# Kernel tuning notes

Measured on AMD Instinct MI355X. Metric: run time of the kernel, lower is better.

## Reference

```python
import jax, jax.numpy as jnp
import numpy as np

B, N, D = 4, 16384, 1024
RANK, NUM_Q = 16, 8
SPARSITY = 0.1
K = max(1, int(N * SPARSITY))  # 1638


def setup_inputs() -> dict:
    key = jax.random.key(0)
    k1, k2, k3 = jax.random.split(key, 3)
    x = jax.random.normal(k1, (B, N, D), dtype=jnp.float32)
    Wk = jax.random.normal(k2, (RANK, D), dtype=jnp.float32)
    queries = jax.random.normal(k3, (NUM_Q, RANK), dtype=jnp.float32)
    return {"x": x, "Wk": Wk, "queries": queries}


def reference(x, Wk, queries):
    # k_proj: [b, n, d] @ [d, rank] -> [b, n, rank]
    keys = jnp.einsum("bnd,rd->bnr", x, Wk)
    # scores: [q, r] x [b, n, r] -> [b, q, n]
    scores = jnp.einsum("qr,bnr->bqn", queries, keys)
    # max over queries -> [b, n]
    token_scores = scores.max(axis=1)
    # eval mode: no jitter noise
    _, indices = jax.lax.top_k(token_scores, K)  # [b, K]
    indices = jnp.sort(indices, axis=-1)
    return indices
```

## Files before the change

kernel.cpp:

```cpp
#include <hip/hip_runtime.h>
#include <stdint.h>

#define B_ 4
#define N_ 16384
#define D_ 1024
#define RANK_ 16
#define NUMQ_ 8
#define KSEL_ 1638

__global__ __launch_bounds__(256) void wq_kernel(const float* __restrict__ Wk,
                                                 const float* __restrict__ queries,
                                                 float* __restrict__ Wq) {
    int i = blockIdx.x * 256 + threadIdx.x;
    if (i >= NUMQ_ * D_) return;
    int q = i >> 10;
    int d = i & (D_ - 1);
    float acc = 0.f;
#pragma unroll
    for (int r = 0; r < RANK_; ++r)
        acc += queries[q * RANK_ + r] * Wk[r * D_ + d];
    Wq[i] = acc;
}

#define TOK 4
__global__ __launch_bounds__(256) void score_kernel(const float* __restrict__ x,
                                                    const float* __restrict__ Wq,
                                                    float* __restrict__ scores) {
    __shared__ float sWq[NUMQ_ * D_];
    for (int i = threadIdx.x; i < NUMQ_ * D_; i += 256)
        sWq[i] = Wq[i];
    __syncthreads();

    const int lane = threadIdx.x & 63;
    const int wave = threadIdx.x >> 6;
    const int gw = blockIdx.x * 4 + wave;
    const int numWaves = gridDim.x * 4;
    const int totalTok = B_ * N_;

    for (int t0 = gw * TOK; t0 < totalTok; t0 += numWaves * TOK) {
        float acc[TOK][NUMQ_];
#pragma unroll
        for (int t = 0; t < TOK; ++t)
#pragma unroll
            for (int q = 0; q < NUMQ_; ++q) acc[t][q] = 0.f;

#pragma unroll
        for (int j = 0; j < 4; ++j) {
            const int off = j * 256 + lane * 4;
            float4 xv[TOK];
#pragma unroll
            for (int t = 0; t < TOK; ++t)
                xv[t] = *(const float4*)(x + (size_t)(t0 + t) * D_ + off);
#pragma unroll
            for (int q = 0; q < NUMQ_; ++q) {
                float4 w = *(const float4*)(sWq + q * D_ + off);
#pragma unroll
                for (int t = 0; t < TOK; ++t) {
                    acc[t][q] += xv[t].x * w.x;
                    acc[t][q] += xv[t].y * w.y;
                    acc[t][q] += xv[t].z * w.z;
                    acc[t][q] += xv[t].w * w.w;
                }
            }
        }

#pragma unroll
        for (int t = 0; t < TOK; ++t) {
            float m = -3.0e38f;
#pragma unroll
            for (int q = 0; q < NUMQ_; ++q) {
                float v = acc[t][q];
#pragma unroll
                for (int s = 32; s > 0; s >>= 1)
                    v += __shfl_xor(v, s, 64);
                m = fmaxf(m, v);
            }
            if (lane == 0) scores[t0 + t] = m;
        }
    }
}

__global__ __launch_bounds__(256) void topk_kernel(const float* __restrict__ scores,
                                                   int* __restrict__ out) {
    __shared__ uint32_t sKeys[N_];
    __shared__ uint32_t hist[256];
    __shared__ uint32_t sGT[256];
    __shared__ uint32_t sEQ[256];
    __shared__ uint32_t sPrefix, sR;

    const int b = blockIdx.x;
    const int tid = threadIdx.x;
    const float* s = scores + b * N_;

    for (int i = tid; i < N_; i += 256) {
        uint32_t u = __float_as_uint(s[i]);
        u = (u & 0x80000000u) ? ~u : (u | 0x80000000u);
        sKeys[i] = u;
    }
    __syncthreads();

    uint32_t prefix = 0;
    uint32_t R = KSEL_;

    for (int shift = 24; shift >= 0; shift -= 8) {
        hist[tid] = 0;
        __syncthreads();
        const uint32_t maskHi = (shift == 24) ? 0u : (0xFFFFFFFFu << (shift + 8));
        for (int i = tid; i < N_; i += 256) {
            uint32_t u = sKeys[i];
            if ((u & maskHi) == prefix)
                atomicAdd(&hist[(u >> shift) & 255u], 1u);
        }
        __syncthreads();
        if (tid == 0) {
            uint32_t cum = 0;
            int sel = 0;
            for (int bin = 255; bin >= 0; --bin) {
                uint32_t c = hist[bin];
                if (cum + c >= R) { sel = bin; break; }
                cum += c;
            }
            sPrefix = prefix | ((uint32_t)sel << shift);
            sR = R - cum;
        }
        __syncthreads();
        prefix = sPrefix;
        R = sR;
        __syncthreads();
    }

    const uint32_t T = prefix;
    const uint32_t need = R;

    const int CHUNK = N_ / 256;
    const int base = tid * CHUNK;
    uint32_t cGT = 0, cEQ = 0;
    for (int i = 0; i < CHUNK; ++i) {
        uint32_t u = sKeys[base + i];
        cGT += (u > T);
        cEQ += (u == T);
    }
    sGT[tid] = cGT;
    sEQ[tid] = cEQ;
    __syncthreads();
    if (tid == 0) {
        uint32_t aG = 0, aE = 0;
        for (int i = 0; i < 256; ++i) {
            uint32_t g = sGT[i], e = sEQ[i];
            sGT[i] = aG; sEQ[i] = aE;
            aG += g; aE += e;
        }
    }
    __syncthreads();

    uint32_t gt = sGT[tid];
    uint32_t eq = sEQ[tid];
    int* ob = out + b * KSEL_;
    for (int i = 0; i < CHUNK; ++i) {
        uint32_t u = sKeys[base + i];
        if (u > T) {
            uint32_t eqSel = (eq < need) ? eq : need;
            ob[gt + eqSel] = base + i;
            gt++;
        } else if (u == T) {
            if (eq < need) ob[gt + eq] = base + i;
            eq++;
        }
    }
}

extern "C" void kernel_launch(void* const* d_in, const int* in_sizes, int n_in,
                              void* d_out, int out_size, void* d_ws, size_t ws_size,
                              hipStream_t stream) {
    const float* x       = (const float*)d_in[0];
    const float* Wk      = (const float*)d_in[1];
    const float* queries = (const float*)d_in[2];
    int* out = (int*)d_out;

    float* Wq     = (float*)d_ws;
    float* scores = (float*)((char*)d_ws + NUMQ_ * D_ * sizeof(float));

    wq_kernel<<<(NUMQ_ * D_ + 255) / 256, 256, 0, stream>>>(Wk, queries, Wq);
    score_kernel<<<2048, 256, 0, stream>>>(x, Wq, scores);
    topk_kernel<<<B_, 256, 0, stream>>>(scores, out);
}
```

Before: 432.5 us.

## Use folded shuffle reduction for scores and 3-pass 11-bit radix select

The score epilogue now uses a transpose-style butterfly fold that halves the live values at each shuffle stage, replacing eight separate full 6-step wave reductions per token. That cuts the shuffle count from 48 to about 13 per token. Top-k selection switches from four 8-bit radix passes to three passes of 11/11/10 bits, using a two-level segment sum to locate the threshold bin. This trades one full histogram pass over shared memory for larger histograms and extra segment-summing work.

```diff
diff --git a/kernel.cpp b/kernel.cpp
--- a/kernel.cpp
+++ b/kernel.cpp
@@ -23,6 +23,14 @@
 }
 
 #define TOK 4
+
+#define FOLD(dst, a, b, bit, dist)                          \
+    {                                                       \
+        float _send = (bit) ? (a) : (b);                    \
+        float _recv = __shfl_xor(_send, (dist), 64);        \
+        (dst) = ((bit) ? (b) : (a)) + _recv;                \
+    }
+
 __global__ __launch_bounds__(256) void score_kernel(const float* __restrict__ x,
                                                     const float* __restrict__ Wq,
                                                     float* __restrict__ scores) {
@@ -36,6 +44,10 @@
     const int gw = blockIdx.x * 4 + wave;
     const int numWaves = gridDim.x * 4;
     const int totalTok = B_ * N_;
+
+    const int l5 = (lane >> 5) & 1;
+    const int l4 = (lane >> 4) & 1;
+    const int l3 = (lane >> 3) & 1;
 
     for (int t0 = gw * TOK; t0 < totalTok; t0 += numWaves * TOK) {
         float acc[TOK][NUMQ_];
@@ -66,16 +78,24 @@
 
 #pragma unroll
         for (int t = 0; t < TOK; ++t) {
-            float m = -3.0e38f;
-#pragma unroll
-            for (int q = 0; q < NUMQ_; ++q) {
-                float v = acc[t][q];
-#pragma unroll
-                for (int s = 32; s > 0; s >>= 1)
-                    v += __shfl_xor(v, s, 64);
-                m = fmaxf(m, v);
-            }
-            if (lane == 0) scores[t0 + t] = m;
+            float n0, n1, n2, n3;
+            FOLD(n0, acc[t][0], acc[t][4], l5, 32)
+            FOLD(n1, acc[t][1], acc[t][5], l5, 32)
+            FOLD(n2, acc[t][2], acc[t][6], l5, 32)
+            FOLD(n3, acc[t][3], acc[t][7], l5, 32)
+            float m0, m1;
+            FOLD(m0, n0, n2, l4, 16)
+            FOLD(m1, n1, n3, l4, 16)
+            float p;
+            FOLD(p, m0, m1, l3, 8)
+            p += __shfl_xor(p, 4, 64);
+            p += __shfl_xor(p, 2, 64);
+            p += __shfl_xor(p, 1, 64);
+            float mx = p;
+            mx = fmaxf(mx, __shfl_xor(mx, 8, 64));
+            mx = fmaxf(mx, __shfl_xor(mx, 16, 64));
+            mx = fmaxf(mx, __shfl_xor(mx, 32, 64));
+            if (lane == 0) scores[t0 + t] = mx;
         }
     }
 }
@@ -83,7 +103,8 @@
 __global__ __launch_bounds__(256) void topk_kernel(const float* __restrict__ scores,
                                                    int* __restrict__ out) {
     __shared__ uint32_t sKeys[N_];
-    __shared__ uint32_t hist[256];
+    __shared__ uint32_t hist[2048];
+    __shared__ uint32_t segSum[256];
     __shared__ uint32_t sGT[256];
     __shared__ uint32_t sEQ[256];
     __shared__ uint32_t sPrefix, sR;
@@ -102,20 +123,42 @@
     uint32_t prefix = 0;
     uint32_t R = KSEL_;
 
-    for (int shift = 24; shift >= 0; shift -= 8) {
-        hist[tid] = 0;
-        __syncthreads();
-        const uint32_t maskHi = (shift == 24) ? 0u : (0xFFFFFFFFu << (shift + 8));
+    const int shifts[3]  = {21, 10, 0};
+    const int widths[3]  = {11, 11, 10};
+
+#pragma unroll 1
+    for (int pass = 0; pass < 3; ++pass) {
+        const int shift = shifts[pass];
+        const uint32_t nb = 1u << widths[pass];
+        const uint32_t binmask = nb - 1u;
+        const uint32_t maskHi = (pass == 0) ? 0u
+                              : (0xFFFFFFFFu << (shift + widths[pass]));
+
+        for (int i = tid; i < (int)nb; i += 256) hist[i] = 0;
+        __syncthreads();
         for (int i = tid; i < N_; i += 256) {
             uint32_t u = sKeys[i];
             if ((u & maskHi) == prefix)
-                atomicAdd(&hist[(u >> shift) & 255u], 1u);
-        }
-        __syncthreads();
+                atomicAdd(&hist[(u >> shift) & binmask], 1u);
+        }
+        __syncthreads();
+
+        const int seg = (int)(nb >> 8);
+        uint32_t ssum = 0;
+        for (int j = 0; j < seg; ++j) ssum += hist[tid * seg + j];
+        segSum[tid] = ssum;
+        __syncthreads();
+
         if (tid == 0) {
             uint32_t cum = 0;
-            int sel = 0;
-            for (int bin = 255; bin >= 0; --bin) {
+            int ts = 0;
+            for (int t2 = 255; t2 >= 0; --t2) {
+                uint32_t c = segSum[t2];
+                if (cum + c >= R) { ts = t2; break; }
+                cum += c;
+            }
+            int sel = ts * seg;
+            for (int bin = ts * seg + seg - 1; bin >= ts * seg; --bin) {
                 uint32_t c = hist[bin];
                 if (cum + c >= R) { sel = bin; break; }
                 cum += c;
```

Result: faster. 410.5 us (-5.1%).
